# Kernel optimization log

Hardware: AMD Instinct MI355X
Metric: run time of the kernel (lower is better)

The kernel has to match this reference:

```python
import jax, jax.numpy as jnp
import numpy as np

D_MODEL = 2048
NUM_HEADS = 16
D_KV = D_MODEL // NUM_HEADS
THETA = 10000.0


def apply_rope(x, pos):
    # x: [B, H, S, d_kv], pos: [S] int
    d = x.shape[-1]
    inv_freq = 1.0 / (THETA ** (jnp.arange(0, d, 2, dtype=jnp.float32) / d))  # [d/2]
    ang = pos.astype(jnp.float32)[:, None] * inv_freq[None, :]  # [S, d/2]
    cos, sin = jnp.cos(ang), jnp.sin(ang)  # broadcast over B,H
    x1 = x[..., 0::2]
    x2 = x[..., 1::2]
    r1 = x1 * cos - x2 * sin
    r2 = x1 * sin + x2 * cos
    return jnp.stack([r1, r2], axis=-1).reshape(x.shape)


def setup_inputs() -> dict:
    key = jax.random.key(0)
    k = jax.random.split(key, 5)
    B, S = 2, 2048
    x = jax.random.normal(k[0], (B, S, D_MODEL), dtype=jnp.float32)
    scale = 1.0 / np.sqrt(D_MODEL)
    Wq = jax.random.normal(k[1], (D_MODEL, D_MODEL), dtype=jnp.float32) * scale
    Wk = jax.random.normal(k[2], (D_MODEL, D_MODEL), dtype=jnp.float32) * scale
    Wv = jax.random.normal(k[3], (D_MODEL, D_MODEL), dtype=jnp.float32) * scale
    Wo = jax.random.normal(k[4], (D_MODEL, D_MODEL), dtype=jnp.float32) * scale
    token_position = jnp.arange(S, dtype=jnp.int64 if jax.config.jax_enable_x64 else jnp.int32)
    return {"x": x, "Wq": Wq, "Wk": Wk, "Wv": Wv, "Wo": Wo, "token_position": token_position}


def reference(x, Wq, Wk, Wv, Wo, token_position):
    B, S, _ = x.shape
    def heads(y):
        return y.reshape(B, S, NUM_HEADS, D_KV).transpose(0, 2, 1, 3)  # [B,H,S,d]
    Q = heads(jnp.einsum('bsd,df->bsf', x, Wq))
    K = heads(jnp.einsum('bsd,df->bsf', x, Wk))
    V = heads(jnp.einsum('bsd,df->bsf', x, Wv))
    Q = apply_rope(Q, token_position)
    K = apply_rope(K, token_position)
    scale = 1.0 / jnp.sqrt(jnp.asarray(D_KV, dtype=x.dtype))
    scores = jnp.einsum('bhqd,bhkd->bhqk', Q, K) * scale  # [B,H,S,S]
    causal = jnp.tril(jnp.ones((S, S), dtype=bool))
    scores = jnp.where(causal, scores, -jnp.inf)
    attn = jax.nn.softmax(scores, axis=-1)
    out = jnp.einsum('bhqk,bhkd->bhqd', attn, V)  # [B,H,S,d]
    out = out.transpose(0, 2, 1, 3).reshape(B, S, D_MODEL)
    return jnp.einsum('bsd,df->bsf', out, Wo)
```

## Files before the change

### kernel.cpp

```cpp
#include <hip/hip_runtime.h>
#include <hip/hip_bf16.h>

#define S 2048
#define DM 2048
#define NH 16
#define DH 128

typedef __attribute__((ext_vector_type(8))) short short8;
typedef __attribute__((ext_vector_type(4))) float floatx4;
typedef unsigned short u16;
typedef unsigned int u32;

__device__ __forceinline__ u16 f2bf(float f) {
  union { float f; u32 u; } v; v.f = f;
  u32 r = v.u + 0x7fffu + ((v.u >> 16) & 1u);
  return (u16)(r >> 16);
}
__device__ __forceinline__ u32 pack2(float lo, float hi) {
  float2 f; f.x = lo; f.y = hi;
  __hip_bfloat162 h = __float22bfloat162_rn(f);
  union { __hip_bfloat162 h; u32 u; } c; c.h = h;
  return c.u;
}

__device__ __forceinline__ floatx4 mfma16(short8 a, short8 b, floatx4 c) {
  return __builtin_amdgcn_mfma_f32_16x16x32_bf16(a, b, c, 0, 0, 0);
}

__device__ __forceinline__ void async_cp16(const u16* g, u16* l) {
  __builtin_amdgcn_global_load_lds(
      (const __attribute__((address_space(1))) void*)g,
      (__attribute__((address_space(3))) void*)l, 16, 0, 0);
}

__global__ void conv_x_k(const float* __restrict__ x, u16* __restrict__ xb) {
  int gid = blockIdx.x * 256 + threadIdx.x;
  float4 v = ((const float4*)x)[gid];
  uint2 p; p.x = pack2(v.x, v.y); p.y = pack2(v.z, v.w);
  ((uint2*)xb)[gid] = p;
}

__global__ void conv_w_k(const float* __restrict__ W0, const float* __restrict__ W1,
                         const float* __restrict__ W2, const float* __restrict__ W3,
                         u16* __restrict__ out) {
  __shared__ float tile[32][33];
  const float* W = blockIdx.z == 0 ? W0 : blockIdx.z == 1 ? W1 : blockIdx.z == 2 ? W2 : W3;
  u16* O = out + (size_t)blockIdx.z * DM * DM;
  int tx = threadIdx.x & 31, ty = threadIdx.x >> 5;
  int k0 = blockIdx.y * 32, n0 = blockIdx.x * 32;
#pragma unroll
  for (int j = 0; j < 4; j++)
    tile[ty + j * 8][tx] = W[(size_t)(k0 + ty + j * 8) * DM + n0 + tx];
  __syncthreads();
#pragma unroll
  for (int j = 0; j < 4; j++)
    O[(size_t)(n0 + ty + j * 8) * DM + k0 + tx] = f2bf(tile[tx][ty + j * 8]);
}

#define BM 256
#define BN 128
#define BK 32
#define NT 64

#define BARRIER __builtin_amdgcn_s_barrier()
#define SB __builtin_amdgcn_sched_barrier(0)
#define LGKM0 asm volatile("s_waitcnt lgkmcnt(0)" ::: "memory")

#define STG_A(q, j, koff) \
  async_cp16(pAg + (size_t)(j) * 64 * DM + (koff), &As[q][soff + (j) * 2048])
#define STG_B(q, j, koff) \
  async_cp16(pBg + (size_t)(j) * 64 * DM + (koff), &Bs[q][soff + (j) * 2048])

#define PH0(p) { \
    a0 = *(const short8*)&As[p][arow + xk]; \
    a1 = *(const short8*)&As[p][arow + 512 + xk]; \
    a2 = *(const short8*)&As[p][arow + 1024 + xk]; \
    a3 = *(const short8*)&As[p][arow + 1536 + xk]; \
    a4 = *(const short8*)&As[p][arow + 2048 + xk]; \
    a5 = *(const short8*)&As[p][arow + 2560 + xk]; \
    a6 = *(const short8*)&As[p][arow + 3072 + xk]; \
    a7 = *(const short8*)&As[p][arow + 3584 + xk]; \
    b0 = *(const short8*)&Bs[p][brow + xk]; \
    b1 = *(const short8*)&Bs[p][brow + 512 + xk]; \
    b2 = *(const short8*)&Bs[p][brow + 1024 + xk]; \
    b3 = *(const short8*)&Bs[p][brow + 1536 + xk]; \
    BARRIER; LGKM0; SB; \
    __builtin_amdgcn_s_setprio(1); \
    acc[0][0] = mfma16(a0, b0, acc[0][0]); \
    acc[1][0] = mfma16(a1, b0, acc[1][0]); \
    acc[2][0] = mfma16(a2, b0, acc[2][0]); \
    acc[3][0] = mfma16(a3, b0, acc[3][0]); \
    acc[0][1] = mfma16(a0, b1, acc[0][1]); \
    acc[1][1] = mfma16(a1, b1, acc[1][1]); \
    acc[2][1] = mfma16(a2, b1, acc[2][1]); \
    acc[3][1] = mfma16(a3, b1, acc[3][1]); \
    acc[0][2] = mfma16(a0, b2, acc[0][2]); \
    acc[1][2] = mfma16(a1, b2, acc[1][2]); \
    acc[2][2] = mfma16(a2, b2, acc[2][2]); \
    acc[3][2] = mfma16(a3, b2, acc[3][2]); \
    acc[0][3] = mfma16(a0, b3, acc[0][3]); \
    acc[1][3] = mfma16(a1, b3, acc[1][3]); \
    acc[2][3] = mfma16(a2, b3, acc[2][3]); \
    acc[3][3] = mfma16(a3, b3, acc[3][3]); \
    __builtin_amdgcn_s_setprio(0); \
    BARRIER; }

#define PH1(p, koff2, PRE2, LAST) { \
    if (PRE2) { STG_B(p, 0, koff2); STG_B(p, 1, koff2); \
                STG_A(p, 0, koff2); STG_A(p, 1, koff2); \
                STG_A(p, 2, koff2); STG_A(p, 3, koff2); } \
    SB; \
    __builtin_amdgcn_s_setprio(1); \
    acc[4][0] = mfma16(a4, b0, acc[4][0]); \
    acc[5][0] = mfma16(a5, b0, acc[5][0]); \
    acc[6][0] = mfma16(a6, b0, acc[6][0]); \
    acc[7][0] = mfma16(a7, b0, acc[7][0]); \
    acc[4][1] = mfma16(a4, b1, acc[4][1]); \
    acc[5][1] = mfma16(a5, b1, acc[5][1]); \
    acc[6][1] = mfma16(a6, b1, acc[6][1]); \
    acc[7][1] = mfma16(a7, b1, acc[7][1]); \
    acc[4][2] = mfma16(a4, b2, acc[4][2]); \
    acc[5][2] = mfma16(a5, b2, acc[5][2]); \
    acc[6][2] = mfma16(a6, b2, acc[6][2]); \
    acc[7][2] = mfma16(a7, b2, acc[7][2]); \
    acc[4][3] = mfma16(a4, b3, acc[4][3]); \
    acc[5][3] = mfma16(a5, b3, acc[5][3]); \
    acc[6][3] = mfma16(a6, b3, acc[6][3]); \
    acc[7][3] = mfma16(a7, b3, acc[7][3]); \
    __builtin_amdgcn_s_setprio(0); SB; \
    if (!LAST) { \
      if (PRE2) { asm volatile("s_waitcnt vmcnt(6)" ::: "memory"); } \
      else      { asm volatile("s_waitcnt vmcnt(0)" ::: "memory"); } \
      BARRIER; SB; } }

__global__ __launch_bounds__(256, 2)
void gemm_k(const u16* __restrict__ A, const u16* __restrict__ Wt,
            u16* __restrict__ oQ, u16* __restrict__ oK, u16* __restrict__ oV,
            const int* __restrict__ tp)
{
  __shared__ u16 As[2][BM * BK];
  __shared__ u16 Bs[2][BN * BK];
  const int t = threadIdx.x;
  const int w = t >> 6, lane = t & 63;
  const int l16 = lane & 15, quad = lane >> 4;
  const int wr = w >> 1, wc = w & 1;
  const int m0 = blockIdx.y * BM, n0 = blockIdx.x * BN;
  const u16* Bt = Wt + (size_t)blockIdx.z * DM * DM;

  const int srow = t >> 2;
  const int sc = ((t & 3) ^ ((t >> 3) & 3)) * 8;
  const u16* pAg = A + (size_t)(m0 + srow) * DM + sc;
  const u16* pBg = Bt + (size_t)(n0 + srow) * DM + sc;
  const int soff = t * 8;

  const int arow = (wr * 128 + l16) * 32;
  const int brow = (wc * 64 + l16) * 32;
  const int xk = ((quad ^ ((l16 >> 1) & 3)) << 3);

  floatx4 acc[8][4] = {};
  short8 a0, a1, a2, a3, a4, a5, a6, a7, b0, b1, b2, b3;

  STG_B(0, 0, 0); STG_B(0, 1, 0);
  STG_A(0, 0, 0); STG_A(0, 1, 0); STG_A(0, 2, 0); STG_A(0, 3, 0);
  STG_B(1, 0, BK); STG_B(1, 1, BK);
  STG_A(1, 0, BK); STG_A(1, 1, BK); STG_A(1, 2, BK); STG_A(1, 3, BK);
  SB;
  asm volatile("s_waitcnt vmcnt(6)" ::: "memory");
  BARRIER; SB;

  for (int it = 0; it < 31; ++it) {
    const int kE = (2 * it + 2) * BK;
    const int kO = (2 * it + 3) * BK;
    PH0(0) PH1(0, kE, 1, 0)
    PH0(1) PH1(1, kO, 1, 0)
  }
  PH0(0) PH1(0, 0, 0, 0)
  PH0(1) PH1(1, 0, 0, 1)

  const int mwb = m0 + wr * 128;
  const int nwb = n0 + wc * 64;
  if ((int)blockIdx.z == 2) {
#pragma unroll
    for (int mi = 0; mi < 8; mi++) {
      int m = mwb + mi * 16 + quad * 4;
      int b = m >> 11, s = m & (S - 1);
#pragma unroll
      for (int ni = 0; ni < 4; ni++) {
        int f = nwb + ni * 16 + l16;
        int h = f >> 7, dh = f & (DH - 1);
        uint2 pk; pk.x = pack2(acc[mi][ni][0], acc[mi][ni][1]);
        pk.y = pack2(acc[mi][ni][2], acc[mi][ni][3]);
        *(uint2*)&oV[((size_t)(b * NH + h) * DH + dh) * S + s] = pk;
      }
    }
  } else {
    u16* Out = ((int)blockIdx.z == 0) ? oQ : oK;
    const float qs = ((int)blockIdx.z == 0) ? 0.12752780f : 1.0f;
#pragma unroll
    for (int mi = 0; mi < 8; mi++) {
#pragma unroll
      for (int r = 0; r < 4; r++) {
        int m = mwb + mi * 16 + quad * 4 + r;
        int b = m >> 11, s = m & (S - 1);
        int ps = tp[s];
#pragma unroll
        for (int ni = 0; ni < 4; ni++) {
          int f = nwb + ni * 16 + l16;
          int h = f >> 7, dh = f & (DH - 1);
          float own = acc[mi][ni][r];
          float oth = __shfl_xor(own, 1, 64);
          float fr = __expf((float)(dh & ~1) * (-9.210340371976184f / 128.0f));
          float ang = (float)ps * fr;
          float sn, cs; __sincosf(ang, &sn, &cs);
          float res = (dh & 1) ? (oth * sn + own * cs) : (own * cs - oth * sn);
          Out[((size_t)(b * NH + h) * S + s) * DH + dh] = f2bf(res * qs);
        }
      }
    }
  }
}

__global__ __launch_bounds__(256, 4)
void oproj_k(const u16* __restrict__ A, const u16* __restrict__ Wt,
             float* __restrict__ oO)
{
  __shared__ u16 As2[128 * 32];
  __shared__ u16 Bs2[128 * 32];
  const int t = threadIdx.x;
  const int w = t >> 6, lane = t & 63;
  const int l16 = lane & 15, quad = lane >> 4;
  const int m0 = blockIdx.y * 128, n0 = blockIdx.x * 128;
  const int wm = (w >> 1) * 64, wn = (w & 1) * 64;
  const u16* Bt = Wt + (size_t)3 * DM * DM;

  const u16* pA[2]; const u16* pB[2]; u16* lA[2]; u16* lB[2];
#pragma unroll
  for (int i = 0; i < 2; i++) {
    int unit = i * 256 + t;
    int row = unit >> 2, s = unit & 3;
    int c = s ^ ((row >> 1) & 3);
    pA[i] = A + (size_t)(m0 + row) * DM + c * 8;
    pB[i] = Bt + (size_t)(n0 + row) * DM + c * 8;
    lA[i] = &As2[unit * 8];
    lB[i] = &Bs2[unit * 8];
  }

  floatx4 acc[4][4] = {};

  for (int k0 = 0; k0 < DM; k0 += 32) {
#pragma unroll
    for (int i = 0; i < 2; i++) {
      async_cp16(pA[i] + k0, lA[i]);
      async_cp16(pB[i] + k0, lB[i]);
    }
    __syncthreads();
    short8 af[4], bfr[4];
#pragma unroll
    for (int i = 0; i < 4; i++) {
      int row = wm + i * 16 + l16;
      af[i] = *(short8*)&As2[(row * 4 + (quad ^ ((row >> 1) & 3))) * 8];
    }
#pragma unroll
    for (int i = 0; i < 4; i++) {
      int row = wn + i * 16 + l16;
      bfr[i] = *(short8*)&Bs2[(row * 4 + (quad ^ ((row >> 1) & 3))) * 8];
    }
#pragma unroll
    for (int mi = 0; mi < 4; mi++)
#pragma unroll
      for (int ni = 0; ni < 4; ni++)
        acc[mi][ni] = mfma16(af[mi], bfr[ni], acc[mi][ni]);
    __syncthreads();
  }

#pragma unroll
  for (int mi = 0; mi < 4; mi++) {
    int m = m0 + wm + mi * 16 + quad * 4;
#pragma unroll
    for (int ni = 0; ni < 4; ni++) {
      int n = n0 + wn + ni * 16 + l16;
#pragma unroll
      for (int r = 0; r < 4; r++)
        oO[(size_t)(m + r) * DM + n] = acc[mi][ni][r];
    }
  }
}

__global__ __launch_bounds__(256, 4)
void attn_k(const u16* __restrict__ Q, const u16* __restrict__ K,
            const u16* __restrict__ Vt, u16* __restrict__ O)
{
  __shared__ u16 Ks[64 * 128];
  __shared__ u16 Vs[128 * 64];
  __shared__ u16 P[4][16 * 64];
  const int t = threadIdx.x, w = t >> 6, lane = t & 63;
  const int l16 = lane & 15, quad = lane >> 4;
  const int task = blockIdx.x;
  const int bh = task & 31, b = bh >> 4, h = bh & 15;
  const int g = 31 - (task >> 5);
  const int qg = g * 64;
  const int qt = qg + w * 16;
  const u16* Qb = Q + (size_t)bh * S * DH;
  const u16* Kb = K + (size_t)bh * S * DH;
  const u16* Vb = Vt + (size_t)bh * DH * S;
  u16* Pw = P[w];
  const int pxor = l16 & 7;

  const u16* pK[4]; u16* lK[4];
  const u16* pV[4]; u16* lV[4];
#pragma unroll
  for (int j = 0; j < 4; j++) {
    int kr = w * 16 + j * 4 + (lane >> 4);
    int ks = lane & 15;
    int kc = ks ^ (kr & 15);
    pK[j] = Kb + (size_t)kr * DH + kc * 8;
    lK[j] = &Ks[kr * 128 + ks * 8];
    int vr = w * 32 + j * 8 + (lane >> 3);
    int vs = lane & 7;
    int vc = vs ^ (vr & 7);
    pV[j] = Vb + (size_t)vr * S + vc * 8;
    lV[j] = &Vs[vr * 64 + vs * 8];
  }

  short8 aq[4];
#pragma unroll
  for (int kc = 0; kc < 4; kc++)
    aq[kc] = *(const short8*)&Qb[(size_t)(qt + l16) * DH + kc * 32 + quad * 8];

  floatx4 o[8] = {};
  float lsum = 0.0f;
  const int kend = qg + 64;

  for (int k0 = 0; k0 < kend; k0 += 64) {
#pragma unroll
    for (int j = 0; j < 4; j++) async_cp16(pK[j] + (size_t)k0 * DH, lK[j]);
#pragma unroll
    for (int j = 0; j < 4; j++) async_cp16(pV[j] + k0, lV[j]);
    __syncthreads();

    floatx4 sc[4] = {};
    __builtin_amdgcn_s_setprio(1);
#pragma unroll
    for (int hh = 0; hh < 4; hh++) {
      int row = hh * 16 + l16;
#pragma unroll
      for (int kc = 0; kc < 4; kc++) {
        short8 kf = *(short8*)&Ks[row * 128 + (((kc * 4 + quad) ^ l16) << 3)];
        sc[hh] = mfma16(kf, aq[kc], sc[hh]);
      }
    }
    __builtin_amdgcn_s_setprio(0);
    if (k0 + 64 > qt) {
#pragma unroll
      for (int hh = 0; hh < 4; hh++)
#pragma unroll
        for (int r = 0; r < 4; r++) {
          int j = k0 + hh * 16 + quad * 4 + r;
          if (j > qt + l16) sc[hh][r] = -3.0e38f;
        }
    }
#pragma unroll
    for (int hh = 0; hh < 4; hh++) {
      float e0 = __builtin_amdgcn_exp2f(fminf(sc[hh][0], 44.0f));
      float e1 = __builtin_amdgcn_exp2f(fminf(sc[hh][1], 44.0f));
      float e2 = __builtin_amdgcn_exp2f(fminf(sc[hh][2], 44.0f));
      float e3 = __builtin_amdgcn_exp2f(fminf(sc[hh][3], 44.0f));
      lsum += (e0 + e1) + (e2 + e3);
      uint2 pk; pk.x = pack2(e0, e1); pk.y = pack2(e2, e3);
      int su = (2 * hh + (quad >> 1)) ^ pxor;
      *(uint2*)&Pw[l16 * 64 + su * 8 + (quad & 1) * 4] = pk;
    }
    asm volatile("s_waitcnt lgkmcnt(0)" ::: "memory");
    __builtin_amdgcn_s_setprio(1);
#pragma unroll
    for (int c = 0; c < 2; c++) {
      short8 pf = *(short8*)&Pw[l16 * 64 + (((4 * c + quad) ^ pxor) << 3)];
#pragma unroll
      for (int t8 = 0; t8 < 8; t8++) {
        int row = t8 * 16 + l16;
        short8 av = *(short8*)&Vs[row * 64 + (((c * 4 + quad) ^ (l16 & 7)) << 3)];
        o[t8] = mfma16(av, pf, o[t8]);
      }
    }
    __builtin_amdgcn_s_setprio(0);
    __syncthreads();
  }

  float l = lsum + __shfl_xor(lsum, 16, 64);
  l += __shfl_xor(l, 32, 64);
  float inv = __builtin_amdgcn_rcpf(l);
#pragma unroll
  for (int t8 = 0; t8 < 8; t8++) {
    uint2 pa;
    pa.x = pack2(o[t8][0] * inv, o[t8][1] * inv);
    pa.y = pack2(o[t8][2] * inv, o[t8][3] * inv);
    *(uint2*)&O[((size_t)(b * S + qt + l16)) * DM + h * DH + t8 * 16 + quad * 4] = pa;
  }
}

extern "C" void kernel_launch(void* const* d_in, const int* in_sizes, int n_in,
                              void* d_out, int out_size, void* d_ws, size_t ws_size,
                              hipStream_t stream) {
  const float* x  = (const float*)d_in[0];
  const float* Wq = (const float*)d_in[1];
  const float* Wk = (const float*)d_in[2];
  const float* Wv = (const float*)d_in[3];
  const float* Wo = (const float*)d_in[4];
  const int*   tp = (const int*)d_in[5];

  char* ws = (char*)d_ws;
  u16* Wt = (u16*)ws;
  u16* xb = (u16*)(ws + 33554432);
  u16* Qb = (u16*)(ws + 50331648);
  u16* Kb = (u16*)(ws + 67108864);
  u16* Vb = (u16*)(ws + 83886080);
  u16* Ob = (u16*)(ws + 100663296);

  conv_x_k<<<8192, 256, 0, stream>>>(x, xb);
  conv_w_k<<<dim3(64, 64, 4), 256, 0, stream>>>(Wq, Wk, Wv, Wo, Wt);
  gemm_k<<<dim3(16, 16, 3), 256, 0, stream>>>(xb, Wt, Qb, Kb, Vb, tp);
  attn_k<<<1024, 256, 0, stream>>>(Qb, Kb, Vb, Ob);
  oproj_k<<<dim3(16, 32), 256, 0, stream>>>(Ob, Wt, (float*)d_out);
}
```

Measured before the change: 378.0 us.

## Double-buffer K/V tiles in attention kernel with async prefetch two tiles ahead

Adds a second shared-memory buffer for the K and V tiles and prefetches tile i+2 while tile i is being computed. Explicit vmcnt waits and barriers replace the load-then-sync pattern, and the loop is unrolled by two to alternate buffers. This aims to hide global-memory latency behind the MFMA work. It doubles K/V LDS use and lowers launch bounds occupancy from 4 to 2 blocks per CU, which may reduce latency hiding across waves.

```diff
diff --git a/kernel.cpp b/kernel.cpp
--- a/kernel.cpp
+++ b/kernel.cpp
@@ -286,12 +286,80 @@
   }
 }
 
-__global__ __launch_bounds__(256, 4)
+#define ATILE(p, i) { \
+    const int k0a = (i) * 64; \
+    floatx4 sc[4] = {}; \
+    __builtin_amdgcn_s_setprio(1); \
+    _Pragma("unroll") \
+    for (int hh = 0; hh < 4; hh++) { \
+      int row = hh * 16 + l16; \
+      _Pragma("unroll") \
+      for (int kc = 0; kc < 4; kc++) { \
+        short8 kf = *(short8*)&Ks[p][row * 128 + (((kc * 4 + quad) ^ l16) << 3)]; \
+        sc[hh] = mfma16(kf, aq[kc], sc[hh]); \
+      } \
+    } \
+    __builtin_amdgcn_s_setprio(0); \
+    if (k0a + 64 > qt) { \
+      _Pragma("unroll") \
+      for (int hh = 0; hh < 4; hh++) \
+        _Pragma("unroll") \
+        for (int r = 0; r < 4; r++) { \
+          int j = k0a + hh * 16 + quad * 4 + r; \
+          if (j > qt + l16) sc[hh][r] = -3.0e38f; \
+        } \
+    } \
+    _Pragma("unroll") \
+    for (int hh = 0; hh < 4; hh++) { \
+      float e0 = __builtin_amdgcn_exp2f(fminf(sc[hh][0], 44.0f)); \
+      float e1 = __builtin_amdgcn_exp2f(fminf(sc[hh][1], 44.0f)); \
+      float e2 = __builtin_amdgcn_exp2f(fminf(sc[hh][2], 44.0f)); \
+      float e3 = __builtin_amdgcn_exp2f(fminf(sc[hh][3], 44.0f)); \
+      lsum += (e0 + e1) + (e2 + e3); \
+      uint2 pk; pk.x = pack2(e0, e1); pk.y = pack2(e2, e3); \
+      int su = (2 * hh + (quad >> 1)) ^ pxor; \
+      *(uint2*)&Pw[l16 * 64 + su * 8 + (quad & 1) * 4] = pk; \
+    } \
+    LGKM0; SB; \
+    BARRIER;                        \
+    if ((i) + 2 < nt) { \
+      _Pragma("unroll") \
+      for (int j = 0; j < 4; j++) \
+        async_cp16(pK[j] + (size_t)(k0a + 128) * DH, &Ks[p][lKo[j]]); \
+    } \
+    __builtin_amdgcn_s_setprio(1); \
+    _Pragma("unroll") \
+    for (int c = 0; c < 2; c++) { \
+      short8 pf = *(short8*)&Pw[l16 * 64 + (((4 * c + quad) ^ pxor) << 3)]; \
+      _Pragma("unroll") \
+      for (int t8 = 0; t8 < 8; t8++) { \
+        int row = t8 * 16 + l16; \
+        short8 av = *(short8*)&Vs[p][row * 64 + (((c * 4 + quad) ^ (l16 & 7)) << 3)]; \
+        o[t8] = mfma16(av, pf, o[t8]); \
+      } \
+    } \
+    __builtin_amdgcn_s_setprio(0); \
+    LGKM0; SB; \
+    BARRIER;                        \
+    if ((i) + 2 < nt) { \
+      _Pragma("unroll") \
+      for (int j = 0; j < 4; j++) \
+        async_cp16(pV[j] + k0a + 128, &Vs[p][lVo[j]]); \
+    } \
+    if ((i) + 1 < nt) { \
+      SB; \
+      if ((i) + 2 < nt) { asm volatile("s_waitcnt vmcnt(8)" ::: "memory"); } \
+      else              { asm volatile("s_waitcnt vmcnt(0)" ::: "memory"); } \
+      BARRIER; SB; \
+    } \
+  }
+
+__global__ __launch_bounds__(256, 2)
 void attn_k(const u16* __restrict__ Q, const u16* __restrict__ K,
             const u16* __restrict__ Vt, u16* __restrict__ O)
 {
-  __shared__ u16 Ks[64 * 128];
-  __shared__ u16 Vs[128 * 64];
+  __shared__ u16 Ks[2][64 * 128];
+  __shared__ u16 Vs[2][128 * 64];
   __shared__ u16 P[4][16 * 64];
   const int t = threadIdx.x, w = t >> 6, lane = t & 63;
   const int l16 = lane & 15, quad = lane >> 4;
@@ -300,26 +368,27 @@
   const int g = 31 - (task >> 5);
   const int qg = g * 64;
   const int qt = qg + w * 16;
+  const int nt = g + 1;
   const u16* Qb = Q + (size_t)bh * S * DH;
   const u16* Kb = K + (size_t)bh * S * DH;
   const u16* Vb = Vt + (size_t)bh * DH * S;
   u16* Pw = P[w];
   const int pxor = l16 & 7;
 
-  const u16* pK[4]; u16* lK[4];
-  const u16* pV[4]; u16* lV[4];
+  const u16* pK[4]; int lKo[4];
+  const u16* pV[4]; int lVo[4];
 #pragma unroll
   for (int j = 0; j < 4; j++) {
-    int kr = w * 16 + j * 4 + (lane >> 4);
-    int ks = lane & 15;
+    int kr = w * 16 + j * 4 + quad;
+    int ks = l16;
     int kc = ks ^ (kr & 15);
     pK[j] = Kb + (size_t)kr * DH + kc * 8;
-    lK[j] = &Ks[kr * 128 + ks * 8];
+    lKo[j] = kr * 128 + ks * 8;
     int vr = w * 32 + j * 8 + (lane >> 3);
     int vs = lane & 7;
     int vc = vs ^ (vr & 7);
     pV[j] = Vb + (size_t)vr * S + vc * 8;
-    lV[j] = &Vs[vr * 64 + vs * 8];
+    lVo[j] = vr * 64 + vs * 8;
   }
 
   short8 aq[4];
@@ -329,62 +398,30 @@
 
   floatx4 o[8] = {};
   float lsum = 0.0f;
-  const int kend = qg + 64;
-
-  for (int k0 = 0; k0 < kend; k0 += 64) {
-#pragma unroll
-    for (int j = 0; j < 4; j++) async_cp16(pK[j] + (size_t)k0 * DH, lK[j]);
-#pragma unroll
-    for (int j = 0; j < 4; j++) async_cp16(pV[j] + k0, lV[j]);
-    __syncthreads();
-
-    floatx4 sc[4] = {};
-    __builtin_amdgcn_s_setprio(1);
-#pragma unroll
-    for (int hh = 0; hh < 4; hh++) {
-      int row = hh * 16 + l16;
-#pragma unroll
-      for (int kc = 0; kc < 4; kc++) {
-        short8 kf = *(short8*)&Ks[row * 128 + (((kc * 4 + quad) ^ l16) << 3)];
-        sc[hh] = mfma16(kf, aq[kc], sc[hh]);
-      }
-    }
-    __builtin_amdgcn_s_setprio(0);
-    if (k0 + 64 > qt) {
-#pragma unroll
-      for (int hh = 0; hh < 4; hh++)
-#pragma unroll
-        for (int r = 0; r < 4; r++) {
-          int j = k0 + hh * 16 + quad * 4 + r;
-          if (j > qt + l16) sc[hh][r] = -3.0e38f;
-        }
-    }
-#pragma unroll
-    for (int hh = 0; hh < 4; hh++) {
-      float e0 = __builtin_amdgcn_exp2f(fminf(sc[hh][0], 44.0f));
-      float e1 = __builtin_amdgcn_exp2f(fminf(sc[hh][1], 44.0f));
-      float e2 = __builtin_amdgcn_exp2f(fminf(sc[hh][2], 44.0f));
-      float e3 = __builtin_amdgcn_exp2f(fminf(sc[hh][3], 44.0f));
-      lsum += (e0 + e1) + (e2 + e3);
-      uint2 pk; pk.x = pack2(e0, e1); pk.y = pack2(e2, e3);
-      int su = (2 * hh + (quad >> 1)) ^ pxor;
-      *(uint2*)&Pw[l16 * 64 + su * 8 + (quad & 1) * 4] = pk;
-    }
-    asm volatile("s_waitcnt lgkmcnt(0)" ::: "memory");
-    __builtin_amdgcn_s_setprio(1);
-#pragma unroll
-    for (int c = 0; c < 2; c++) {
-      short8 pf = *(short8*)&Pw[l16 * 64 + (((4 * c + quad) ^ pxor) << 3)];
-#pragma unroll
-      for (int t8 = 0; t8 < 8; t8++) {
-        int row = t8 * 16 + l16;
-        short8 av = *(short8*)&Vs[row * 64 + (((c * 4 + quad) ^ (l16 & 7)) << 3)];
-        o[t8] = mfma16(av, pf, o[t8]);
-      }
-    }
-    __builtin_amdgcn_s_setprio(0);
-    __syncthreads();
-  }
+
+#pragma unroll
+  for (int j = 0; j < 4; j++) async_cp16(pK[j], &Ks[0][lKo[j]]);
+#pragma unroll
+  for (int j = 0; j < 4; j++) async_cp16(pV[j], &Vs[0][lVo[j]]);
+  if (nt > 1) {
+#pragma unroll
+    for (int j = 0; j < 4; j++) async_cp16(pK[j] + (size_t)64 * DH, &Ks[1][lKo[j]]);
+#pragma unroll
+    for (int j = 0; j < 4; j++) async_cp16(pV[j] + 64, &Vs[1][lVo[j]]);
+    SB;
+    asm volatile("s_waitcnt vmcnt(8)" ::: "memory");
+  } else {
+    SB;
+    asm volatile("s_waitcnt vmcnt(0)" ::: "memory");
+  }
+  BARRIER; SB;
+
+  int i = 0;
+  for (; i + 2 <= nt; i += 2) {
+    ATILE(0, i)
+    ATILE(1, i + 1)
+  }
+  if (i < nt) { ATILE(0, i) }
 
   float l = lsum + __shfl_xor(lsum, 16, 64);
   l += __shfl_xor(l, 32, 64);
```

Result: faster. 369.3 us (-2.3%).
